# Kernel optimization log

Measured on AMD Instinct MI355X. Metric: run time of the kernel, lower is better.

The kernel has to match this reference:

```python
import jax, jax.numpy as jnp
import numpy as np
from jax import lax

B, N_ENT, D_ENT = 64, 512, 256
C_SCAT, C_MAP, W = 32, 18, 64
N_RES = 4


def conv2d(x, w, stride, pad):
    return lax.conv_general_dilated(x, w, (stride, stride), [(pad, pad), (pad, pad)],
                                    dimension_numbers=('NCHW', 'OIHW', 'NCHW'))


def batchnorm(x, g, b, eps=1e-5):
    # training-mode BN (batch statistics), matching nn.BatchNorm2d default train()
    mu = x.mean((0, 2, 3), keepdims=True)
    var = x.var((0, 2, 3), keepdims=True)
    return g[None, :, None, None] * (x - mu) * lax.rsqrt(var + eps) + b[None, :, None, None]


def setup_inputs() -> dict:
    key = jax.random.key(0)
    ks = jax.random.split(key, 24)
    s = 0.05
    inp = {
        'x': jax.random.uniform(ks[0], (B, C_MAP, W, W), jnp.float32),
        'entity_embeddings': jax.random.normal(ks[1], (B, N_ENT, D_ENT), jnp.float32),
        'entity_x_y': jax.random.randint(ks[2], (B, N_ENT, 16), 0, 2, jnp.int32),
        'conv1_w': jax.random.normal(ks[3], (C_SCAT, D_ENT), jnp.float32) * s,
        'project_w': jax.random.normal(ks[4], (32, C_SCAT + C_MAP, 1, 1), jnp.float32) * s,
        'project_b': jnp.zeros((32,), jnp.float32),
        'ds1_w': jax.random.normal(ks[5], (64, 32, 4, 4), jnp.float32) * s,
        'ds1_b': jnp.zeros((64,), jnp.float32),
        'ds2_w': jax.random.normal(ks[6], (128, 64, 4, 4), jnp.float32) * s,
        'ds2_b': jnp.zeros((128,), jnp.float32),
        'ds3_w': jax.random.normal(ks[7], (128, 128, 4, 4), jnp.float32) * s,
        'ds3_b': jnp.zeros((128,), jnp.float32),
        'res_conv1_w': jax.random.normal(ks[8], (N_RES, 128, 128, 3, 3), jnp.float32) * s,
        'res_bn1_g': jnp.ones((N_RES, 128), jnp.float32),
        'res_bn1_b': jnp.zeros((N_RES, 128), jnp.float32),
        'res_conv2_w': jax.random.normal(ks[9], (N_RES, 128, 128, 3, 3), jnp.float32) * s,
        'res_bn2_g': jnp.ones((N_RES, 128), jnp.float32),
        'res_bn2_b': jnp.zeros((N_RES, 128), jnp.float32),
        'fc_w': jax.random.normal(ks[10], (256, 8 * 8 * 128), jnp.float32) * s,
        'fc_b': jnp.zeros((256,), jnp.float32),
    }
    return inp


def _scatter(entity_embeddings, entity_x_y, conv1_w):
    # reduced = relu(Conv1d(256->32, k=1)) on entity dim
    reduced = jax.nn.relu(jnp.einsum('bnd,cd->bnc', entity_embeddings, conv1_w))  # [B,N,32]
    bits = entity_x_y
    pow2 = (2 ** jnp.arange(7, -1, -1)).astype(jnp.int32)
    xv = (bits[..., :8] * pow2).sum(-1) // 4   # [B,N] in 0..63
    yv = (bits[..., 8:] * pow2).sum(-1) // 4
    valid = (bits[..., 0] != -1000000000)
    reduced = reduced * valid[..., None].astype(reduced.dtype)
    b_idx = jnp.arange(entity_embeddings.shape[0], dtype=jnp.int32)[:, None]
    flat = (b_idx * (W * W) + yv * W + xv).reshape(-1)
    scat = jax.ops.segment_sum(reduced.reshape(-1, C_SCAT), flat, num_segments=entity_embeddings.shape[0] * W * W)
    return scat.reshape(-1, W, W, C_SCAT).transpose(0, 3, 1, 2)  # [B,32,W,W]


def reference(x, entity_embeddings, entity_x_y, conv1_w, project_w, project_b,
              ds1_w, ds1_b, ds2_w, ds2_b, ds3_w, ds3_b,
              res_conv1_w, res_bn1_g, res_bn1_b, res_conv2_w, res_bn2_g, res_bn2_b,
              fc_w, fc_b):
    scatter_map = _scatter(entity_embeddings, entity_x_y, conv1_w)
    h = jnp.concatenate([scatter_map, x], axis=1)  # [B,50,64,64]
    h = jax.nn.relu(conv2d(h, project_w, 1, 0) + project_b[None, :, None, None])
    h = jax.nn.relu(conv2d(h, ds1_w, 2, 1) + ds1_b[None, :, None, None])   # [B,64,32,32]
    h = jax.nn.relu(conv2d(h, ds2_w, 2, 1) + ds2_b[None, :, None, None])   # [B,128,16,16]
    h = jax.nn.relu(conv2d(h, ds3_w, 2, 1) + ds3_b[None, :, None, None])   # [B,128,8,8]
    map_skip = h
    for i in range(N_RES):
        identity = h
        o = batchnorm(conv2d(h, res_conv1_w[i], 1, 1), res_bn1_g[i], res_bn1_b[i])
        o = jax.nn.relu(o)
        o = batchnorm(conv2d(o, res_conv2_w[i], 1, 1), res_bn2_g[i], res_bn2_b[i])
        h = jax.nn.relu(o + identity)
        map_skip = map_skip + h
    flat = h.reshape(h.shape[0], -1)
    embedded_spatial = jax.nn.relu(flat @ fc_w.T + fc_b)
    return (map_skip, embedded_spatial)
```

## Files before the change

kernel.cpp:

```cpp
#include <hip/hip_runtime.h>
#include <hip/hip_bf16.h>

typedef __attribute__((ext_vector_type(8))) short bf16x8;
typedef __attribute__((ext_vector_type(4))) short bf16x4;
typedef __attribute__((ext_vector_type(4))) float f32x4;

__device__ __forceinline__ short f2bs(float v) {
  __hip_bfloat16 h = __float2bfloat16(v);
  return *reinterpret_cast<short*>(&h);
}

__global__ __launch_bounds__(256) void k_wall(
    const float* __restrict__ rc1w, const float* __restrict__ rc2w,
    const float* __restrict__ d1w, const float* __restrict__ d2w,
    const float* __restrict__ d3w, const float* __restrict__ fcw,
    const float* __restrict__ c1w, const float* __restrict__ pw,
    short* __restrict__ wTr1, short* __restrict__ wTr2, short* __restrict__ wTds1,
    short* __restrict__ wTds2, short* __restrict__ wTds3, short* __restrict__ wfcbf,
    short* __restrict__ wsc, short* __restrict__ wproj) {
  __shared__ float ld[128 * 65];
  const int bx = blockIdx.x;
  const int tid = threadIdx.x;
  if (bx < 4608) {
    const float* src = (bx < 2304) ? rc1w : rc2w;
    short* dst = (bx < 2304) ? wTr1 : wTr2;
    const int i = (bx % 2304) * 256 + tid;
    if (i < 589824) {
      const int layer = i / 147456;
      const int rem = i % 147456;
      const int tap = rem / 16384;
      const int r2 = rem & 16383;
      const int co = r2 >> 7, ci = r2 & 127;
      dst[i] = f2bs(src[(((size_t)layer * 16384 + co * 128 + ci) * 9) + tap]);
    }
  } else if (bx < 6272) {
    int CIN, n, base;
    const float* src;
    short* dst;
    if (bx < 4736) { CIN = 32; n = 32768; base = 4608; src = d1w; dst = wTds1; }
    else if (bx < 5248) { CIN = 64; n = 131072; base = 4736; src = d2w; dst = wTds2; }
    else { CIN = 128; n = 262144; base = 5248; src = d3w; dst = wTds3; }
    const int i = (bx - base) * 256 + tid;
    if (i < n) {
      const int COCI = n / 16;
      const int tap = i / COCI;
      const int rem = i % COCI;
      dst[i] = f2bs(src[(size_t)rem * 16 + tap]);
    }
  } else if (bx < 6528) {
    const int j = bx - 6272;
    const float* sp = fcw + (size_t)j * 8192;
    for (int i = tid; i < 8192; i += 256) {
      const int co = i >> 6, pix = i & 63;
      ld[co * 65 + pix] = sp[i];
    }
    __syncthreads();
    short* dp = wfcbf + (size_t)j * 8192;
    for (int i = tid; i < 8192; i += 256) {
      const int pix = i >> 7, co = i & 127;
      dp[i] = f2bs(ld[co * 65 + pix]);
    }
  } else if (bx < 6560) {
    const int i = (bx - 6528) * 256 + tid;
    if (i < 8192) wsc[i] = f2bs(c1w[i]);
  } else {
    const int i = (bx - 6560) * 256 + tid;
    if (i < 2048) {
      const int co = i >> 6, k = i & 63;
      wproj[i] = (k < 50) ? f2bs(pw[co * 50 + k]) : (short)0;
    }
  }
}

__global__ __launch_bounds__(256) void k_scatmfma(const float* __restrict__ emb,
                                                  const int* __restrict__ xy,
                                                  const short* __restrict__ wsc,
                                                  float* __restrict__ scat_pm) {
  constexpr int CIP = 264;
  __shared__ short abf[64 * CIP];
  __shared__ int flat[64];
  const int tid = threadIdx.x;
  const int e0 = blockIdx.x * 64;
  const float4* eg = (const float4*)(emb + (size_t)e0 * 256);
  for (int i = tid; i < 4096; i += 256) {
    const int e = i >> 6, k4 = i & 63;
    const float4 v = eg[(size_t)e * 64 + k4];
    bf16x4 o;
    o[0] = f2bs(v.x); o[1] = f2bs(v.y); o[2] = f2bs(v.z); o[3] = f2bs(v.w);
    *(bf16x4*)(&abf[e * CIP + k4 * 4]) = o;
  }
  if (tid < 64) {
    const int* bp = xy + (size_t)(e0 + tid) * 16;
    int xv = 0, yv = 0;
#pragma unroll
    for (int j = 0; j < 8; ++j) xv = (xv << 1) | bp[j];
#pragma unroll
    for (int j = 8; j < 16; ++j) yv = (yv << 1) | bp[j];
    flat[tid] = (bp[0] != -1000000000)
                    ? (((e0 + tid) >> 9) * 4096 + ((yv >> 2) << 6) + (xv >> 2))
                    : -1;
  }
  __syncthreads();
  const int wq = __builtin_amdgcn_readfirstlane(tid >> 6);
  const int lane = tid & 63;
  const int l15 = lane & 15, quad = lane >> 4;
  f32x4 acc[2];
  acc[0] = (f32x4){0.f, 0.f, 0.f, 0.f};
  acc[1] = (f32x4){0.f, 0.f, 0.f, 0.f};
  const short* arow = &abf[(wq * 16 + l15) * CIP + quad * 8];
  const short* w0 = wsc + (size_t)l15 * 256 + quad * 8;
  const short* w1 = wsc + (size_t)(16 + l15) * 256 + quad * 8;
#pragma unroll
  for (int kk = 0; kk < 8; ++kk) {
    bf16x8 a = *(const bf16x8*)(arow + kk * 32);
    acc[0] = __builtin_amdgcn_mfma_f32_16x16x32_bf16(a, *(const bf16x8*)(w0 + kk * 32), acc[0], 0, 0, 0);
    acc[1] = __builtin_amdgcn_mfma_f32_16x16x32_bf16(a, *(const bf16x8*)(w1 + kk * 32), acc[1], 0, 0, 0);
  }
#pragma unroll
  for (int nt = 0; nt < 2; ++nt)
#pragma unroll
    for (int r = 0; r < 4; ++r) {
      const int e = wq * 16 + quad * 4 + r;
      const float v = acc[nt][r];
      const int f = flat[e];
      if (f >= 0 && v > 0.f)
        atomicAdd(&scat_pm[(size_t)f * 32 + nt * 16 + l15], v);
    }
}

__global__ __launch_bounds__(256) void k_projmfma(const float* __restrict__ scat_pm,
                                                  const float* __restrict__ xin,
                                                  const short* __restrict__ wproj,
                                                  const float* __restrict__ pb,
                                                  short* __restrict__ h0pm) {
  constexpr int PK = 72;
  __shared__ short abf[128 * PK];
  const int tid = threadIdx.x;
  const int b = blockIdx.x >> 5;
  const int yx0 = (blockIdx.x & 31) << 7;
  const float4* sg = (const float4*)(scat_pm + ((size_t)(b * 4096 + yx0)) * 32);
  for (int i = tid; i < 1024; i += 256) {
    const int p = i >> 3, c4 = i & 7;
    const float4 v = sg[(size_t)p * 8 + c4];
    bf16x4 o;
    o[0] = f2bs(v.x); o[1] = f2bs(v.y); o[2] = f2bs(v.z); o[3] = f2bs(v.w);
    *(bf16x4*)(&abf[p * PK + c4 * 4]) = o;
  }
  for (int i = tid; i < 2304; i += 256) {
    const int run = i >> 7, p = i & 127;
    abf[p * PK + 32 + run] = f2bs(xin[(size_t)(b * 18 + run) * 4096 + yx0 + p]);
  }
  for (int i = tid; i < 2048; i += 256) {
    const int p = i >> 4, k = 50 + (i & 15);
    abf[p * PK + k] = 0;
  }
  __syncthreads();
  const int wq = __builtin_amdgcn_readfirstlane(tid >> 6);
  const int lane = tid & 63;
  const int l15 = lane & 15, quad = lane >> 4;
  f32x4 acc[2][2];
#pragma unroll
  for (int t = 0; t < 2; ++t)
#pragma unroll
    for (int n = 0; n < 2; ++n) acc[t][n] = (f32x4){0.f, 0.f, 0.f, 0.f};
  const short* wb0 = wproj + (size_t)l15 * 64 + quad * 8;
  const short* wb1 = wproj + (size_t)(16 + l15) * 64 + quad * 8;
#pragma unroll
  for (int kk = 0; kk < 2; ++kk) {
    const bf16x8 b0 = *(const bf16x8*)(wb0 + kk * 32);
    const bf16x8 b1 = *(const bf16x8*)(wb1 + kk * 32);
#pragma unroll
    for (int t = 0; t < 2; ++t) {
      const int pix = (wq * 2 + t) * 16 + l15;
      bf16x8 a = *(const bf16x8*)(&abf[pix * PK + quad * 8 + kk * 32]);
      acc[t][0] = __builtin_amdgcn_mfma_f32_16x16x32_bf16(a, b0, acc[t][0], 0, 0, 0);
      acc[t][1] = __builtin_amdgcn_mfma_f32_16x16x32_bf16(a, b1, acc[t][1], 0, 0, 0);
    }
  }
#pragma unroll
  for (int t = 0; t < 2; ++t)
#pragma unroll
    for (int n = 0; n < 2; ++n) {
      const int co = n * 16 + l15;
      const float bv = pb[co];
#pragma unroll
      for (int r = 0; r < 4; ++r) {
        const int pix = (wq * 2 + t) * 16 + quad * 4 + r;
        float v = acc[t][n][r] + bv;
        v = v > 0.f ? v : 0.f;
        h0pm[((size_t)(b * 4096 + yx0 + pix)) * 32 + co] = f2bs(v);
      }
    }
}

template <int CIN, int COUT, int HIN, int ROWSO, int COSPLIT, int MT, int NT, int OUTMODE>
__global__ __launch_bounds__(256) void k_ds2(const short* __restrict__ inpm,
                                             const short* __restrict__ wT,
                                             const float* __restrict__ bias,
                                             short* __restrict__ outbf,
                                             float* __restrict__ outf,
                                             float* __restrict__ msf) {
  constexpr int HOUT = HIN / 2;
  constexpr int ROWS = 2 * ROWSO + 2;
  constexpr int COLS = HIN + 2;
  constexpr int CHUNKS = CIN / 8;
  constexpr int KK = CIN / 32;
  constexpr int CIPAD = CIN + 8;
  constexpr int NHO = HOUT / ROWSO;
  __shared__ short lin[ROWS * COLS * CIPAD];
  const int tid = threadIdx.x;
  int bx = blockIdx.x;
  const int co_blk = (COSPLIT > 1) ? (bx % COSPLIT) : 0;
  if (COSPLIT > 1) bx /= COSPLIT;
  const int hoblk = bx % NHO;
  const int b = bx / NHO;
  for (int i = tid; i < ROWS * COLS * CHUNKS; i += 256) {
    const int ch = i % CHUNKS;
    const int pixv = i / CHUNKS;
    const int r = pixv / COLS, c = pixv % COLS;
    const int hi = 2 * ROWSO * hoblk - 1 + r;
    const int wc = c - 1;
    bf16x8 v = (bf16x8)(short)0;
    if (hi >= 0 && hi < HIN && wc >= 0 && wc < HIN)
      v = *(const bf16x8*)(inpm + ((size_t)(b * HIN + hi) * HIN + wc) * CIN + ch * 8);
    *(bf16x8*)(&lin[(r * COLS + c) * CIPAD + ch * 8]) = v;
  }
  __syncthreads();
  const int wq = __builtin_amdgcn_readfirstlane(tid >> 6);
  const int lane = tid & 63;
  const int l15 = lane & 15, quad = lane >> 4;
  const int mtile = (MT > 1) ? (wq % MT) : 0;
  const int cogrp = wq / MT;
  const int cobase = co_blk * (COUT / COSPLIT) + cogrp * (NT * 16);
  const int p = mtile * 16 + l15;
  const int dr = p / HOUT;
  const int col = p % HOUT;
  f32x4 acc[NT];
#pragma unroll
  for (int n = 0; n < NT; ++n) acc[n] = (f32x4){0.f, 0.f, 0.f, 0.f};
  const short* wrow = wT + (size_t)(cobase + l15) * CIN + quad * 8;
  for (int ky = 0; ky < 4; ++ky) {
    for (int kx = 0; kx < 4; ++kx) {
      const short* arow = &lin[((2 * dr + ky) * COLS + 2 * col + kx) * CIPAD + quad * 8];
      const short* wt = wrow + (size_t)(ky * 4 + kx) * COUT * CIN;
#pragma unroll
      for (int kk = 0; kk < KK; ++kk) {
        bf16x8 a = *(const bf16x8*)(arow + kk * 32);
#pragma unroll
        for (int n = 0; n < NT; ++n) {
          bf16x8 bf = *(const bf16x8*)(wt + n * 16 * CIN + kk * 32);
          acc[n] = __builtin_amdgcn_mfma_f32_16x16x32_bf16(a, bf, acc[n], 0, 0, 0);
        }
      }
    }
  }
#pragma unroll
  for (int n = 0; n < NT; ++n) {
    const int co = cobase + n * 16 + l15;
    const float bv = bias[co];
#pragma unroll
    for (int r = 0; r < 4; ++r) {
      const int pp = mtile * 16 + quad * 4 + r;
      const int dr2 = pp / HOUT;
      const int c2 = pp % HOUT;
      const int ho = hoblk * ROWSO + dr2;
      float v = acc[n][r] + bv;
      v = v > 0.f ? v : 0.f;
      const size_t o = ((size_t)b * HOUT * HOUT + ho * HOUT + c2) * COUT + co;
      outbf[o] = f2bs(v);
      if (OUTMODE == 1) {
        outf[o] = v;
        msf[o] = v;
      }
    }
  }
}

template <int BNIN>
__global__ __launch_bounds__(256) void k_resmfma(const short* __restrict__ hbfin,
                                                 const float* __restrict__ fin,
                                                 const float* __restrict__ statsIn,
                                                 const float* __restrict__ gIn,
                                                 const float* __restrict__ bIn,
                                                 const short* __restrict__ wT,
                                                 float* __restrict__ outpm,
                                                 float* __restrict__ statsOut) {
  constexpr int CIPAD = 136;
  __shared__ short lin[100 * CIPAD];
  __shared__ float bnsc[128], bnsh[128];
  const int tid = threadIdx.x;
  const int b = blockIdx.x >> 3;
  const int cobase = (blockIdx.x & 7) << 4;
  if (BNIN == 1) {
    if (tid < 128) {
      const float mu = statsIn[tid] * (1.f / 4096.f);
      const float var = statsIn[128 + tid] * (1.f / 4096.f) - mu * mu;
      const float sc = gIn[tid] * rsqrtf(var + 1e-5f);
      bnsc[tid] = sc;
      bnsh[tid] = bIn[tid] - mu * sc;
    }
    __syncthreads();
  }
  if (BNIN == 0) {
    const short* hb = hbfin + ((size_t)b << 13);
    for (int i = tid; i < 1600; i += 256) {
      const int pixel = i >> 4, ch = i & 15;
      const int r = pixel / 10, c = pixel % 10;
      bf16x8 v = (bf16x8)(short)0;
      if (r >= 1 && r <= 8 && c >= 1 && c <= 8)
        v = *(const bf16x8*)(hb + (((r - 1) << 3) + (c - 1)) * 128 + ch * 8);
      *(bf16x8*)(&lin[pixel * CIPAD + ch * 8]) = v;
    }
  } else {
    const float* fb = fin + ((size_t)b << 13);
    for (int i = tid; i < 3200; i += 256) {
      const int pixel = i >> 5, c4 = i & 31;
      const int r = pixel / 10, c = pixel % 10;
      bf16x4 o = (bf16x4)(short)0;
      if (r >= 1 && r <= 8 && c >= 1 && c <= 8) {
        const float4 x = *(const float4*)(fb + (size_t)(((r - 1) << 3) + (c - 1)) * 128 + c4 * 4);
        const float xv[4] = {x.x, x.y, x.z, x.w};
#pragma unroll
        for (int k = 0; k < 4; ++k) {
          const int ci = c4 * 4 + k;
          const float v = xv[k] * bnsc[ci] + bnsh[ci];
          o[k] = f2bs(v > 0.f ? v : 0.f);
        }
      }
      *(bf16x4*)(&lin[pixel * CIPAD + c4 * 4]) = o;
    }
  }
  __syncthreads();
  const int wq = __builtin_amdgcn_readfirstlane(tid >> 6);
  const int lane = tid & 63;
  const int l15 = lane & 15, quad = lane >> 4;
  const int p = wq * 16 + l15;
  const int py = p >> 3, px = p & 7;
  f32x4 acc = (f32x4){0.f, 0.f, 0.f, 0.f};
  const short* wrow = wT + (size_t)(cobase + l15) * 128 + quad * 8;
  for (int t = 0; t < 9; ++t) {
    const int ky = t / 3, kx = t % 3;
    const short* arow = &lin[((py + ky) * 10 + px + kx) * CIPAD + quad * 8];
    const short* wt = wrow + (size_t)t * 16384;
#pragma unroll
    for (int kk = 0; kk < 4; ++kk) {
      bf16x8 a = *(const bf16x8*)(arow + kk * 32);
      bf16x8 bf = *(const bf16x8*)(wt + kk * 32);
      acc = __builtin_amdgcn_mfma_f32_16x16x32_bf16(a, bf, acc, 0, 0, 0);
    }
  }
  float* ob = outpm + ((size_t)b << 13);
  const int co = cobase + l15;
  float s = 0.f, q = 0.f;
#pragma unroll
  for (int r = 0; r < 4; ++r) {
    const float v = acc[r];
    ob[(size_t)(wq * 16 + quad * 4 + r) * 128 + co] = v;
    s += v;
    q += v * v;
  }
  s += __shfl_down(s, 32); q += __shfl_down(q, 32);
  s += __shfl_down(s, 16); q += __shfl_down(q, 16);
  if (lane < 16) {
    atomicAdd(&statsOut[co], s);
    atomicAdd(&statsOut[128 + co], q);
  }
}

__global__ __launch_bounds__(256) void k_bnadd(const float* __restrict__ inpm,
                                               const float* __restrict__ stats,
                                               const float* __restrict__ g,
                                               const float* __restrict__ bb,
                                               const float* __restrict__ identpm,
                                               float* __restrict__ houtpm,
                                               short* __restrict__ houtbf,
                                               float* __restrict__ mspm) {
  const int idx = blockIdx.x * 256 + threadIdx.x;
  const int co = idx & 127;
  const float mu = stats[co] * (1.f / 4096.f);
  const float var = stats[128 + co] * (1.f / 4096.f) - mu * mu;
  float v = g[co] * (inpm[idx] - mu) * rsqrtf(var + 1e-5f) + bb[co];
  v += identpm[idx];
  v = v > 0.f ? v : 0.f;
  houtpm[idx] = v;
  houtbf[idx] = f2bs(v);
  mspm[idx] += v;
}

__global__ __launch_bounds__(256) void k_mstrans(const float* __restrict__ mspm,
                                                 float* __restrict__ out0) {
  __shared__ float t[64 * 132];
  const int b = blockIdx.x;
  const int tid = threadIdx.x;
  const float* sp = mspm + ((size_t)b << 13);
  for (int i = tid; i < 8192; i += 256) {
    const int pix = i >> 7, co = i & 127;
    t[pix * 132 + co] = sp[i];
  }
  __syncthreads();
  float* dp = out0 + ((size_t)b << 13);
  for (int i = tid; i < 8192; i += 256) {
    const int co = i >> 6, pix = i & 63;
    dp[i] = t[pix * 132 + co];
  }
}

__global__ __launch_bounds__(256) void k_fcmfma(const short* __restrict__ hbf,
                                                const short* __restrict__ wbf,
                                                float* __restrict__ part) {
  const int nb = blockIdx.x & 3;
  const int kb = blockIdx.x >> 2;
  const int wq = __builtin_amdgcn_readfirstlane((int)(threadIdx.x >> 6));
  const int lane = threadIdx.x & 63;
  const int l15 = lane & 15, quad = lane >> 4;
  const int k0 = kb * 256 + quad * 8;
  const short* wp = wbf + (size_t)(nb * 64 + wq * 16 + l15) * 8192 + k0;
  const short* hp = hbf + (size_t)l15 * 8192 + k0;
  f32x4 acc[4];
#pragma unroll
  for (int m = 0; m < 4; ++m) acc[m] = (f32x4){0.f, 0.f, 0.f, 0.f};
  for (int ks = 0; ks < 8; ++ks) {
    bf16x8 bfr = *(const bf16x8*)(wp + ks * 32);
#pragma unroll
    for (int m = 0; m < 4; ++m) {
      bf16x8 a = *(const bf16x8*)(hp + (size_t)m * 16 * 8192 + ks * 32);
      acc[m] = __builtin_amdgcn_mfma_f32_16x16x32_bf16(a, bfr, acc[m], 0, 0, 0);
    }
  }
#pragma unroll
  for (int m = 0; m < 4; ++m)
#pragma unroll
    for (int r = 0; r < 4; ++r) {
      const int b = m * 16 + quad * 4 + r;
      part[((size_t)kb * 64 + b) * 256 + nb * 64 + wq * 16 + l15] = acc[m][r];
    }
}

__global__ __launch_bounds__(256) void k_fcred(const float* __restrict__ part,
                                               const float* __restrict__ bias,
                                               float* __restrict__ out1) {
  const int idx = blockIdx.x * 256 + threadIdx.x;
  const int j = idx & 255;
  float s = 0.f;
#pragma unroll 8
  for (int kb = 0; kb < 32; ++kb) s += part[(size_t)kb * 16384 + idx];
  const float v = s + bias[j];
  out1[idx] = v > 0.f ? v : 0.f;
}

extern "C" void kernel_launch(void* const* d_in, const int* in_sizes, int n_in,
                              void* d_out, int out_size, void* d_ws, size_t ws_size,
                              hipStream_t stream) {
  const float* xin = (const float*)d_in[0];
  const float* emb = (const float*)d_in[1];
  const int* xy = (const int*)d_in[2];
  const float* c1w = (const float*)d_in[3];
  const float* pw = (const float*)d_in[4];
  const float* pb = (const float*)d_in[5];
  const float* d1w = (const float*)d_in[6];
  const float* d1b = (const float*)d_in[7];
  const float* d2w = (const float*)d_in[8];
  const float* d2b = (const float*)d_in[9];
  const float* d3w = (const float*)d_in[10];
  const float* d3b = (const float*)d_in[11];
  const float* rc1w = (const float*)d_in[12];
  const float* rbn1g = (const float*)d_in[13];
  const float* rbn1b = (const float*)d_in[14];
  const float* rc2w = (const float*)d_in[15];
  const float* rbn2g = (const float*)d_in[16];
  const float* rbn2b = (const float*)d_in[17];
  const float* fcw = (const float*)d_in[18];
  const float* fcb = (const float*)d_in[19];

  float* out0 = (float*)d_out;
  float* out1 = out0 + 524288;

  float* F = (float*)d_ws;
  float* scat = F + 0;
  float* h1pm_f = F + 0;
  float* h2pm_f = F + 2097152;
  float* hApm = F + 3145728;
  float* hBpm = F + 3670016;
  float* tmppm = F + 4194304;
  float* tmp2pm = F + 4718592;
  float* mspm = F + 5242880;
  short* pmbfA = (short*)(F + 5767168);
  short* pmbfB = (short*)(F + 6029312);
  float* stats = F + 6291456;
  float* fcpart = F + 6293504;
  short* h0pm = (short*)(F + 8388608);
  short* wfcbf = (short*)(F + 12582912);
  short* wTr1 = (short*)(F + 13631488);
  short* wTr2 = wTr1 + 589824;
  short* wTds1 = wTr2 + 589824;
  short* wTds2 = wTds1 + 32768;
  short* wTds3 = wTds2 + 131072;
  short* wsc = wTds3 + 262144;
  short* wproj = wsc + 8192;

  hipMemsetAsync(scat, 0, 8388608 * sizeof(float), stream);
  k_wall<<<6568, 256, 0, stream>>>(rc1w, rc2w, d1w, d2w, d3w, fcw, c1w, pw,
                                   wTr1, wTr2, wTds1, wTds2, wTds3, wfcbf, wsc, wproj);
  k_scatmfma<<<512, 256, 0, stream>>>(emb, xy, wsc, scat);
  k_projmfma<<<2048, 256, 0, stream>>>(scat, xin, wproj, pb, h0pm);
  hipMemsetAsync(stats, 0, 2048 * sizeof(float), stream);
  short* h1pm = (short*)h1pm_f;
  short* h2pm = (short*)h2pm_f;
  k_ds2<32, 64, 64, 2, 1, 4, 4, 0><<<1024, 256, 0, stream>>>(h0pm, wTds1, d1b, h1pm, hApm, mspm);
  k_ds2<64, 128, 32, 1, 1, 1, 2, 0><<<1024, 256, 0, stream>>>(h1pm, wTds2, d2b, h2pm, hApm, mspm);
  k_ds2<128, 128, 16, 2, 2, 1, 1, 1><<<512, 256, 0, stream>>>(h2pm, wTds3, d3b, pmbfA, hApm, mspm);

  float* cur = hApm;  float* nxt = hBpm;
  short* curbf = pmbfA; short* nxtbf = pmbfB;
  for (int i = 0; i < 4; ++i) {
    float* sA = stats + i * 512;
    float* sB = stats + i * 512 + 256;
    k_resmfma<0><<<512, 256, 0, stream>>>(curbf, nullptr, nullptr, nullptr, nullptr,
                                          wTr1 + (size_t)i * 147456, tmppm, sA);
    k_resmfma<1><<<512, 256, 0, stream>>>(nullptr, tmppm, sA, rbn1g + i * 128, rbn1b + i * 128,
                                          wTr2 + (size_t)i * 147456, tmp2pm, sB);
    k_bnadd<<<2048, 256, 0, stream>>>(tmp2pm, sB, rbn2g + i * 128, rbn2b + i * 128, cur, nxt,
                                      nxtbf, mspm);
    float* sw = cur; cur = nxt; nxt = sw;
    short* swb = curbf; curbf = nxtbf; nxtbf = swb;
  }
  k_mstrans<<<64, 256, 0, stream>>>(mspm, out0);
  k_fcmfma<<<128, 256, 0, stream>>>(curbf, wfcbf, fcpart);
  k_fcred<<<64, 256, 0, stream>>>(fcpart, fcb, out1);
}
```

Measured before the change: 409.5 us.

## Fuse downsample, residual, and FC stages into one persistent kernel with grid barriers

Replaces the chain of ds, resmfma, bnadd, mstrans and fc launches with a single persistent 512-block kernel. The stages are separated by atomic-counter grid barriers, and the residual identity and map_skip sums stay in registers. The BN2 output is applied straight from the accumulator, which drops the tmp2, bnadd and mstrans round trips and about twenty kernel launches. In exchange it relies on all 512 blocks being co-resident, which launch_bounds(256,2) is meant to allow, and it adds spin-wait barrier cost at each phase.

```diff
diff --git a/kernel.cpp b/kernel.cpp
--- a/kernel.cpp
+++ b/kernel.cpp
@@ -193,13 +193,24 @@
     }
 }
 
-template <int CIN, int COUT, int HIN, int ROWSO, int COSPLIT, int MT, int NT, int OUTMODE>
-__global__ __launch_bounds__(256) void k_ds2(const short* __restrict__ inpm,
-                                             const short* __restrict__ wT,
-                                             const float* __restrict__ bias,
-                                             short* __restrict__ outbf,
-                                             float* __restrict__ outf,
-                                             float* __restrict__ msf) {
+__device__ __forceinline__ void gbar(unsigned* cnt, unsigned target) {
+  __syncthreads();
+  if (threadIdx.x == 0) {
+    __threadfence();
+    __hip_atomic_fetch_add(cnt, 1u, __ATOMIC_RELEASE, __HIP_MEMORY_SCOPE_AGENT);
+    while (__hip_atomic_load(cnt, __ATOMIC_RELAXED, __HIP_MEMORY_SCOPE_AGENT) < target)
+      __builtin_amdgcn_s_sleep(1);
+    __threadfence();
+  }
+  __syncthreads();
+}
+
+template <int CIN, int COUT, int HIN, int ROWSO, int COSPLIT, int MT, int NT, int WRF32>
+__device__ __forceinline__ void ds2_phase(int bx, const short* __restrict__ inpm,
+                                          const short* __restrict__ wT,
+                                          const float* __restrict__ bias,
+                                          short* __restrict__ outbf,
+                                          float* __restrict__ outf, short* lin) {
   constexpr int HOUT = HIN / 2;
   constexpr int ROWS = 2 * ROWSO + 2;
   constexpr int COLS = HIN + 2;
@@ -207,13 +218,12 @@
   constexpr int KK = CIN / 32;
   constexpr int CIPAD = CIN + 8;
   constexpr int NHO = HOUT / ROWSO;
-  __shared__ short lin[ROWS * COLS * CIPAD];
   const int tid = threadIdx.x;
-  int bx = blockIdx.x;
   const int co_blk = (COSPLIT > 1) ? (bx % COSPLIT) : 0;
   if (COSPLIT > 1) bx /= COSPLIT;
   const int hoblk = bx % NHO;
   const int b = bx / NHO;
+  __syncthreads();
   for (int i = tid; i < ROWS * COLS * CHUNKS; i += 256) {
     const int ch = i % CHUNKS;
     const int pixv = i / CHUNKS;
@@ -268,79 +278,20 @@
       v = v > 0.f ? v : 0.f;
       const size_t o = ((size_t)b * HOUT * HOUT + ho * HOUT + c2) * COUT + co;
       outbf[o] = f2bs(v);
-      if (OUTMODE == 1) {
-        outf[o] = v;
-        msf[o] = v;
-      }
-    }
-  }
-}
-
-template <int BNIN>
-__global__ __launch_bounds__(256) void k_resmfma(const short* __restrict__ hbfin,
-                                                 const float* __restrict__ fin,
-                                                 const float* __restrict__ statsIn,
-                                                 const float* __restrict__ gIn,
-                                                 const float* __restrict__ bIn,
-                                                 const short* __restrict__ wT,
-                                                 float* __restrict__ outpm,
-                                                 float* __restrict__ statsOut) {
-  constexpr int CIPAD = 136;
-  __shared__ short lin[100 * CIPAD];
-  __shared__ float bnsc[128], bnsh[128];
-  const int tid = threadIdx.x;
-  const int b = blockIdx.x >> 3;
-  const int cobase = (blockIdx.x & 7) << 4;
-  if (BNIN == 1) {
-    if (tid < 128) {
-      const float mu = statsIn[tid] * (1.f / 4096.f);
-      const float var = statsIn[128 + tid] * (1.f / 4096.f) - mu * mu;
-      const float sc = gIn[tid] * rsqrtf(var + 1e-5f);
-      bnsc[tid] = sc;
-      bnsh[tid] = bIn[tid] - mu * sc;
-    }
-    __syncthreads();
-  }
-  if (BNIN == 0) {
-    const short* hb = hbfin + ((size_t)b << 13);
-    for (int i = tid; i < 1600; i += 256) {
-      const int pixel = i >> 4, ch = i & 15;
-      const int r = pixel / 10, c = pixel % 10;
-      bf16x8 v = (bf16x8)(short)0;
-      if (r >= 1 && r <= 8 && c >= 1 && c <= 8)
-        v = *(const bf16x8*)(hb + (((r - 1) << 3) + (c - 1)) * 128 + ch * 8);
-      *(bf16x8*)(&lin[pixel * CIPAD + ch * 8]) = v;
-    }
-  } else {
-    const float* fb = fin + ((size_t)b << 13);
-    for (int i = tid; i < 3200; i += 256) {
-      const int pixel = i >> 5, c4 = i & 31;
-      const int r = pixel / 10, c = pixel % 10;
-      bf16x4 o = (bf16x4)(short)0;
-      if (r >= 1 && r <= 8 && c >= 1 && c <= 8) {
-        const float4 x = *(const float4*)(fb + (size_t)(((r - 1) << 3) + (c - 1)) * 128 + c4 * 4);
-        const float xv[4] = {x.x, x.y, x.z, x.w};
-#pragma unroll
-        for (int k = 0; k < 4; ++k) {
-          const int ci = c4 * 4 + k;
-          const float v = xv[k] * bnsc[ci] + bnsh[ci];
-          o[k] = f2bs(v > 0.f ? v : 0.f);
-        }
-      }
-      *(bf16x4*)(&lin[pixel * CIPAD + c4 * 4]) = o;
-    }
-  }
-  __syncthreads();
-  const int wq = __builtin_amdgcn_readfirstlane(tid >> 6);
-  const int lane = tid & 63;
-  const int l15 = lane & 15, quad = lane >> 4;
+      if (WRF32) outf[o] = v;
+    }
+  }
+}
+
+__device__ __forceinline__ f32x4 res_mfma(const short* lin, const short* __restrict__ wT,
+                                          int cobase, int wq, int l15, int quad) {
   const int p = wq * 16 + l15;
   const int py = p >> 3, px = p & 7;
   f32x4 acc = (f32x4){0.f, 0.f, 0.f, 0.f};
   const short* wrow = wT + (size_t)(cobase + l15) * 128 + quad * 8;
   for (int t = 0; t < 9; ++t) {
     const int ky = t / 3, kx = t % 3;
-    const short* arow = &lin[((py + ky) * 10 + px + kx) * CIPAD + quad * 8];
+    const short* arow = &lin[((py + ky) * 10 + px + kx) * 136 + quad * 8];
     const short* wt = wrow + (size_t)t * 16384;
 #pragma unroll
     for (int kk = 0; kk < 4; ++kk) {
@@ -349,103 +300,173 @@
       acc = __builtin_amdgcn_mfma_f32_16x16x32_bf16(a, bf, acc, 0, 0, 0);
     }
   }
-  float* ob = outpm + ((size_t)b << 13);
+  return acc;
+}
+
+__global__ __launch_bounds__(256, 2) void k_tail(
+    const short* __restrict__ h0pm,
+    const short* __restrict__ wTds1, const float* __restrict__ d1b, short* __restrict__ h1pm,
+    const short* __restrict__ wTds2, const float* __restrict__ d2b, short* __restrict__ h2pm,
+    const short* __restrict__ wTds3, const float* __restrict__ d3b,
+    short* __restrict__ hbf, float* __restrict__ hf32, float* __restrict__ tmppm,
+    const short* __restrict__ wTr1, const short* __restrict__ wTr2,
+    const float* __restrict__ rbn1g, const float* __restrict__ rbn1b,
+    const float* __restrict__ rbn2g, const float* __restrict__ rbn2b,
+    float* __restrict__ stats, unsigned* __restrict__ cnt,
+    const short* __restrict__ wfc, const float* __restrict__ fcb,
+    float* __restrict__ fcpart, float* __restrict__ out0, float* __restrict__ out1) {
+  __shared__ short smem[15840];
+  const int bid = blockIdx.x;
+  const int tid = threadIdx.x;
+  unsigned ph = 0;
+
+  ds2_phase<32, 64, 64, 2, 1, 4, 4, 0>(bid, h0pm, wTds1, d1b, h1pm, nullptr, smem);
+  ds2_phase<32, 64, 64, 2, 1, 4, 4, 0>(bid + 512, h0pm, wTds1, d1b, h1pm, nullptr, smem);
+  gbar(cnt, 512u * (++ph));
+  ds2_phase<64, 128, 32, 1, 1, 1, 2, 0>(bid, h1pm, wTds2, d2b, h2pm, nullptr, smem);
+  ds2_phase<64, 128, 32, 1, 1, 1, 2, 0>(bid + 512, h1pm, wTds2, d2b, h2pm, nullptr, smem);
+  gbar(cnt, 512u * (++ph));
+  ds2_phase<128, 128, 16, 2, 2, 1, 1, 1>(bid, h2pm, wTds3, d3b, hbf, hf32, smem);
+  gbar(cnt, 512u * (++ph));
+
+  const int b = bid >> 3;
+  const int cobase = (bid & 7) << 4;
+  const int wq = __builtin_amdgcn_readfirstlane(tid >> 6);
+  const int lane = tid & 63;
+  const int l15 = lane & 15, quad = lane >> 4;
   const int co = cobase + l15;
-  float s = 0.f, q = 0.f;
-#pragma unroll
-  for (int r = 0; r < 4; ++r) {
-    const float v = acc[r];
-    ob[(size_t)(wq * 16 + quad * 4 + r) * 128 + co] = v;
-    s += v;
-    q += v * v;
-  }
-  s += __shfl_down(s, 32); q += __shfl_down(q, 32);
-  s += __shfl_down(s, 16); q += __shfl_down(q, 16);
-  if (lane < 16) {
-    atomicAdd(&statsOut[co], s);
-    atomicAdd(&statsOut[128 + co], q);
-  }
-}
-
-__global__ __launch_bounds__(256) void k_bnadd(const float* __restrict__ inpm,
-                                               const float* __restrict__ stats,
-                                               const float* __restrict__ g,
-                                               const float* __restrict__ bb,
-                                               const float* __restrict__ identpm,
-                                               float* __restrict__ houtpm,
-                                               short* __restrict__ houtbf,
-                                               float* __restrict__ mspm) {
-  const int idx = blockIdx.x * 256 + threadIdx.x;
-  const int co = idx & 127;
-  const float mu = stats[co] * (1.f / 4096.f);
-  const float var = stats[128 + co] * (1.f / 4096.f) - mu * mu;
-  float v = g[co] * (inpm[idx] - mu) * rsqrtf(var + 1e-5f) + bb[co];
-  v += identpm[idx];
-  v = v > 0.f ? v : 0.f;
-  houtpm[idx] = v;
-  houtbf[idx] = f2bs(v);
-  mspm[idx] += v;
-}
-
-__global__ __launch_bounds__(256) void k_mstrans(const float* __restrict__ mspm,
-                                                 float* __restrict__ out0) {
-  __shared__ float t[64 * 132];
-  const int b = blockIdx.x;
-  const int tid = threadIdx.x;
-  const float* sp = mspm + ((size_t)b << 13);
-  for (int i = tid; i < 8192; i += 256) {
-    const int pix = i >> 7, co = i & 127;
-    t[pix * 132 + co] = sp[i];
-  }
-  __syncthreads();
-  float* dp = out0 + ((size_t)b << 13);
-  for (int i = tid; i < 8192; i += 256) {
-    const int co = i >> 6, pix = i & 63;
-    dp[i] = t[pix * 132 + co];
-  }
-}
-
-__global__ __launch_bounds__(256) void k_fcmfma(const short* __restrict__ hbf,
-                                                const short* __restrict__ wbf,
-                                                float* __restrict__ part) {
-  const int nb = blockIdx.x & 3;
-  const int kb = blockIdx.x >> 2;
-  const int wq = __builtin_amdgcn_readfirstlane((int)(threadIdx.x >> 6));
-  const int lane = threadIdx.x & 63;
-  const int l15 = lane & 15, quad = lane >> 4;
-  const int k0 = kb * 256 + quad * 8;
-  const short* wp = wbf + (size_t)(nb * 64 + wq * 16 + l15) * 8192 + k0;
-  const short* hp = hbf + (size_t)l15 * 8192 + k0;
-  f32x4 acc[4];
-#pragma unroll
-  for (int m = 0; m < 4; ++m) acc[m] = (f32x4){0.f, 0.f, 0.f, 0.f};
-  for (int ks = 0; ks < 8; ++ks) {
-    bf16x8 bfr = *(const bf16x8*)(wp + ks * 32);
-#pragma unroll
-    for (int m = 0; m < 4; ++m) {
-      bf16x8 a = *(const bf16x8*)(hp + (size_t)m * 16 * 8192 + ks * 32);
-      acc[m] = __builtin_amdgcn_mfma_f32_16x16x32_bf16(a, bfr, acc[m], 0, 0, 0);
-    }
-  }
-#pragma unroll
-  for (int m = 0; m < 4; ++m)
+  float hloc[4], msloc[4];
+  {
+    const float* hf = hf32 + ((size_t)b << 13);
 #pragma unroll
     for (int r = 0; r < 4; ++r) {
-      const int b = m * 16 + quad * 4 + r;
-      part[((size_t)kb * 64 + b) * 256 + nb * 64 + wq * 16 + l15] = acc[m][r];
-    }
-}
-
-__global__ __launch_bounds__(256) void k_fcred(const float* __restrict__ part,
-                                               const float* __restrict__ bias,
-                                               float* __restrict__ out1) {
-  const int idx = blockIdx.x * 256 + threadIdx.x;
-  const int j = idx & 255;
-  float s = 0.f;
+      hloc[r] = hf[(size_t)(wq * 16 + quad * 4 + r) * 128 + co];
+      msloc[r] = hloc[r];
+    }
+  }
+  float* const bnsc = (float*)(smem + 13600);
+  float* const bnsh = bnsc + 128;
+
+  for (int i = 0; i < 4; ++i) {
+    float* sA = stats + i * 512;
+    float* sB = sA + 256;
+    {
+      __syncthreads();
+      const short* hb = hbf + ((size_t)b << 13);
+      for (int t = tid; t < 1600; t += 256) {
+        const int pixel = t >> 4, ch = t & 15;
+        const int r = pixel / 10, c = pixel % 10;
+        bf16x8 v = (bf16x8)(short)0;
+        if (r >= 1 && r <= 8 && c >= 1 && c <= 8)
+          v = *(const bf16x8*)(hb + (((r - 1) << 3) + (c - 1)) * 128 + ch * 8);
+        *(bf16x8*)(&smem[pixel * 136 + ch * 8]) = v;
+      }
+      __syncthreads();
+      f32x4 acc = res_mfma(smem, wTr1 + (size_t)i * 147456, cobase, wq, l15, quad);
+      float* ob = tmppm + ((size_t)b << 13);
+      float s = 0.f, q = 0.f;
+#pragma unroll
+      for (int r = 0; r < 4; ++r) {
+        const float v = acc[r];
+        ob[(size_t)(wq * 16 + quad * 4 + r) * 128 + co] = v;
+        s += v; q += v * v;
+      }
+      s += __shfl_down(s, 32); q += __shfl_down(q, 32);
+      s += __shfl_down(s, 16); q += __shfl_down(q, 16);
+      if (lane < 16) {
+        atomicAdd(&sA[cobase + lane], s);
+        atomicAdd(&sA[128 + cobase + lane], q);
+      }
+    }
+    gbar(cnt, 512u * (++ph));
+    f32x4 acc2;
+    {
+      __syncthreads();
+      if (tid < 128) {
+        const float mu = sA[tid] * (1.f / 4096.f);
+        const float var = sA[128 + tid] * (1.f / 4096.f) - mu * mu;
+        const float sc = rbn1g[i * 128 + tid] * rsqrtf(var + 1e-5f);
+        bnsc[tid] = sc;
+        bnsh[tid] = rbn1b[i * 128 + tid] - mu * sc;
+      }
+      __syncthreads();
+      const float* fb = tmppm + ((size_t)b << 13);
+      for (int t = tid; t < 3200; t += 256) {
+        const int pixel = t >> 5, c4 = t & 31;
+        const int r = pixel / 10, c = pixel % 10;
+        bf16x4 o = (bf16x4)(short)0;
+        if (r >= 1 && r <= 8 && c >= 1 && c <= 8) {
+          const float4 x = *(const float4*)(fb + (size_t)(((r - 1) << 3) + (c - 1)) * 128 + c4 * 4);
+          const float xv[4] = {x.x, x.y, x.z, x.w};
+#pragma unroll
+          for (int k2 = 0; k2 < 4; ++k2) {
+            const int ci = c4 * 4 + k2;
+            const float v = xv[k2] * bnsc[ci] + bnsh[ci];
+            o[k2] = f2bs(v > 0.f ? v : 0.f);
+          }
+        }
+        *(bf16x4*)(&smem[pixel * 136 + c4 * 4]) = o;
+      }
+      __syncthreads();
+      acc2 = res_mfma(smem, wTr2 + (size_t)i * 147456, cobase, wq, l15, quad);
+      float s = 0.f, q = 0.f;
+#pragma unroll
+      for (int r = 0; r < 4; ++r) { s += acc2[r]; q += acc2[r] * acc2[r]; }
+      s += __shfl_down(s, 32); q += __shfl_down(q, 32);
+      s += __shfl_down(s, 16); q += __shfl_down(q, 16);
+      if (lane < 16) {
+        atomicAdd(&sB[cobase + lane], s);
+        atomicAdd(&sB[128 + cobase + lane], q);
+      }
+    }
+    gbar(cnt, 512u * (++ph));
+    {
+      const float mu = sB[co] * (1.f / 4096.f);
+      const float var = sB[128 + co] * (1.f / 4096.f) - mu * mu;
+      const float sc = rbn2g[i * 128 + co] * rsqrtf(var + 1e-5f);
+      const float sh = rbn2b[i * 128 + co] - mu * sc;
+      short* hb = hbf + ((size_t)b << 13);
+#pragma unroll
+      for (int r = 0; r < 4; ++r) {
+        float v = acc2[r] * sc + sh + hloc[r];
+        v = v > 0.f ? v : 0.f;
+        hloc[r] = v;
+        msloc[r] += v;
+        hb[(size_t)(wq * 16 + quad * 4 + r) * 128 + co] = f2bs(v);
+      }
+    }
+    gbar(cnt, 512u * (++ph));
+  }
+
+  {
+    float* ob = out0 + ((size_t)b << 13) + (size_t)co * 64;
+#pragma unroll
+    for (int r = 0; r < 4; ++r) ob[wq * 16 + quad * 4 + r] = msloc[r];
+  }
+
+  {
+    const int kb = bid >> 4, jb = bid & 15;
+    const int k0 = kb * 256 + quad * 8;
+    const short* hp = hbf + (size_t)(wq * 16 + l15) * 8192 + k0;
+    const short* wp = wfc + (size_t)(jb * 16 + l15) * 8192 + k0;
+    f32x4 acc = (f32x4){0.f, 0.f, 0.f, 0.f};
+#pragma unroll
+    for (int ks = 0; ks < 8; ++ks)
+      acc = __builtin_amdgcn_mfma_f32_16x16x32_bf16(*(const bf16x8*)(hp + ks * 32),
+                                                    *(const bf16x8*)(wp + ks * 32), acc, 0, 0, 0);
+#pragma unroll
+    for (int r = 0; r < 4; ++r)
+      fcpart[((size_t)kb * 64 + wq * 16 + quad * 4 + r) * 256 + jb * 16 + l15] = acc[r];
+  }
+  gbar(cnt, 512u * (++ph));
+  if (bid < 64) {
+    const int idx = bid * 256 + tid;
+    float s = 0.f;
 #pragma unroll 8
-  for (int kb = 0; kb < 32; ++kb) s += part[(size_t)kb * 16384 + idx];
-  const float v = s + bias[j];
-  out1[idx] = v > 0.f ? v : 0.f;
+    for (int kb2 = 0; kb2 < 32; ++kb2) s += fcpart[(size_t)kb2 * 16384 + idx];
+    const float v = s + fcb[idx & 255];
+    out1[idx] = v > 0.f ? v : 0.f;
+  }
 }
 
 extern "C" void kernel_launch(void* const* d_in, const int* in_sizes, int n_in,
@@ -477,17 +498,14 @@
 
   float* F = (float*)d_ws;
   float* scat = F + 0;
-  float* h1pm_f = F + 0;
-  float* h2pm_f = F + 2097152;
-  float* hApm = F + 3145728;
-  float* hBpm = F + 3670016;
+  short* h1pm = (short*)(F + 0);
+  short* h2pm = (short*)(F + 2097152);
+  float* hf32 = F + 3145728;
   float* tmppm = F + 4194304;
-  float* tmp2pm = F + 4718592;
-  float* mspm = F + 5242880;
-  short* pmbfA = (short*)(F + 5767168);
-  short* pmbfB = (short*)(F + 6029312);
+  short* hbf = (short*)(F + 5767168);
   float* stats = F + 6291456;
-  float* fcpart = F + 6293504;
+  unsigned* cnt = (unsigned*)(F + 6293504);
+  float* fcpart = F + 6293568;
   short* h0pm = (short*)(F + 8388608);
   short* wfcbf = (short*)(F + 12582912);
   short* wTr1 = (short*)(F + 13631488);
@@ -503,28 +521,8 @@
                                    wTr1, wTr2, wTds1, wTds2, wTds3, wfcbf, wsc, wproj);
   k_scatmfma<<<512, 256, 0, stream>>>(emb, xy, wsc, scat);
   k_projmfma<<<2048, 256, 0, stream>>>(scat, xin, wproj, pb, h0pm);
-  hipMemsetAsync(stats, 0, 2048 * sizeof(float), stream);
-  short* h1pm = (short*)h1pm_f;
-  short* h2pm = (short*)h2pm_f;
-  k_ds2<32, 64, 64, 2, 1, 4, 4, 0><<<1024, 256, 0, stream>>>(h0pm, wTds1, d1b, h1pm, hApm, mspm);
-  k_ds2<64, 128, 32, 1, 1, 1, 2, 0><<<1024, 256, 0, stream>>>(h1pm, wTds2, d2b, h2pm, hApm, mspm);
-  k_ds2<128, 128, 16, 2, 2, 1, 1, 1><<<512, 256, 0, stream>>>(h2pm, wTds3, d3b, pmbfA, hApm, mspm);
-
-  float* cur = hApm;  float* nxt = hBpm;
-  short* curbf = pmbfA; short* nxtbf = pmbfB;
-  for (int i = 0; i < 4; ++i) {
-    float* sA = stats + i * 512;
-    float* sB = stats + i * 512 + 256;
-    k_resmfma<0><<<512, 256, 0, stream>>>(curbf, nullptr, nullptr, nullptr, nullptr,
-                                          wTr1 + (size_t)i * 147456, tmppm, sA);
-    k_resmfma<1><<<512, 256, 0, stream>>>(nullptr, tmppm, sA, rbn1g + i * 128, rbn1b + i * 128,
-                                          wTr2 + (size_t)i * 147456, tmp2pm, sB);
-    k_bnadd<<<2048, 256, 0, stream>>>(tmp2pm, sB, rbn2g + i * 128, rbn2b + i * 128, cur, nxt,
-                                      nxtbf, mspm);
-    float* sw = cur; cur = nxt; nxt = sw;
-    short* swb = curbf; curbf = nxtbf; nxtbf = swb;
-  }
-  k_mstrans<<<64, 256, 0, stream>>>(mspm, out0);
-  k_fcmfma<<<128, 256, 0, stream>>>(curbf, wfcbf, fcpart);
-  k_fcred<<<64, 256, 0, stream>>>(fcpart, fcb, out1);
-}
+  hipMemsetAsync(stats, 0, (2048 + 16) * sizeof(float), stream);
+  k_tail<<<512, 256, 0, stream>>>(h0pm, wTds1, d1b, h1pm, wTds2, d2b, h2pm, wTds3, d3b,
+                                  hbf, hf32, tmppm, wTr1, wTr2, rbn1g, rbn1b, rbn2g, rbn2b,
+                                  stats, cnt, wfcbf, fcb, fcpart, out0, out1);
+}
```

Result: slower. 1.256 ms (+206.8%).

## Fuse residual BN-add into next conv and fold memsets into weight prep

Applied to the files above, without the earlier changes.

Folds the two hipMemsetAsync calls into extra blocks of the weight-conversion kernel. The separate BN2+residual+ReLU kernel is fused into the next block's first 3x3 conv, which now applies BN2 while staging its halo tile into LDS. The final BN-add is fused into the map_skip transpose kernel, which also emits the bf16 input for the FC. The aim is fewer launches and less round-trip global traffic. In exchange, each conv block recomputes the BN-add for its whole image tile, and ownership of the fp32 writes is split across the 8 channel blocks.

```diff
diff --git a/kernel.cpp b/kernel.cpp
--- a/kernel.cpp
+++ b/kernel.cpp
@@ -17,7 +17,8 @@
     const float* __restrict__ c1w, const float* __restrict__ pw,
     short* __restrict__ wTr1, short* __restrict__ wTr2, short* __restrict__ wTds1,
     short* __restrict__ wTds2, short* __restrict__ wTds3, short* __restrict__ wfcbf,
-    short* __restrict__ wsc, short* __restrict__ wproj) {
+    short* __restrict__ wsc, short* __restrict__ wproj,
+    float* __restrict__ scatz, float* __restrict__ statsz) {
   __shared__ float ld[128 * 65];
   const int bx = blockIdx.x;
   const int tid = threadIdx.x;
@@ -63,12 +64,18 @@
   } else if (bx < 6560) {
     const int i = (bx - 6528) * 256 + tid;
     if (i < 8192) wsc[i] = f2bs(c1w[i]);
-  } else {
+  } else if (bx < 6568) {
     const int i = (bx - 6560) * 256 + tid;
     if (i < 2048) {
       const int co = i >> 6, k = i & 63;
       wproj[i] = (k < 50) ? f2bs(pw[co * 50 + k]) : (short)0;
     }
+  } else if (bx < 7080) {
+    float4* dst = (float4*)(scatz + (size_t)(bx - 6568) * 16384);
+    const float4 z = {0.f, 0.f, 0.f, 0.f};
+    for (int t = tid; t < 4096; t += 256) dst[t] = z;
+  } else {
+    for (int i = tid; i < 2064; i += 256) statsz[i] = 0.f;
   }
 }
 
@@ -367,41 +374,129 @@
   }
 }
 
-__global__ __launch_bounds__(256) void k_bnadd(const float* __restrict__ inpm,
-                                               const float* __restrict__ stats,
-                                               const float* __restrict__ g,
-                                               const float* __restrict__ bb,
-                                               const float* __restrict__ identpm,
-                                               float* __restrict__ houtpm,
-                                               short* __restrict__ houtbf,
-                                               float* __restrict__ mspm) {
-  const int idx = blockIdx.x * 256 + threadIdx.x;
-  const int co = idx & 127;
-  const float mu = stats[co] * (1.f / 4096.f);
-  const float var = stats[128 + co] * (1.f / 4096.f) - mu * mu;
-  float v = g[co] * (inpm[idx] - mu) * rsqrtf(var + 1e-5f) + bb[co];
-  v += identpm[idx];
-  v = v > 0.f ? v : 0.f;
-  houtpm[idx] = v;
-  houtbf[idx] = f2bs(v);
-  mspm[idx] += v;
-}
-
-__global__ __launch_bounds__(256) void k_mstrans(const float* __restrict__ mspm,
-                                                 float* __restrict__ out0) {
+__global__ __launch_bounds__(256) void k_resA(const float* __restrict__ tmp2,
+                                              const float* __restrict__ statsB,
+                                              const float* __restrict__ g2,
+                                              const float* __restrict__ b2,
+                                              const float* __restrict__ identf,
+                                              float* __restrict__ houtf,
+                                              float* __restrict__ mspm,
+                                              const short* __restrict__ wT,
+                                              float* __restrict__ outpm,
+                                              float* __restrict__ statsOut) {
+  constexpr int CIPAD = 136;
+  __shared__ short lin[100 * CIPAD];
+  __shared__ float bnsc[128], bnsh[128];
+  const int tid = threadIdx.x;
+  const int b = blockIdx.x >> 3;
+  const int cobase = (blockIdx.x & 7) << 4;
+  if (tid < 128) {
+    const float mu = statsB[tid] * (1.f / 4096.f);
+    const float var = statsB[128 + tid] * (1.f / 4096.f) - mu * mu;
+    const float sc = g2[tid] * rsqrtf(var + 1e-5f);
+    bnsc[tid] = sc;
+    bnsh[tid] = b2[tid] - mu * sc;
+  }
+  __syncthreads();
+  const float* fb = tmp2 + ((size_t)b << 13);
+  const float* idb = identf + ((size_t)b << 13);
+  for (int t = tid; t < 3200; t += 256) {
+    const int pixel = t >> 5, c4 = t & 31;
+    const int r = pixel / 10, c = pixel % 10;
+    bf16x4 o = (bf16x4)(short)0;
+    if (r >= 1 && r <= 8 && c >= 1 && c <= 8) {
+      const size_t p8 = (size_t)(((r - 1) << 3) + (c - 1)) * 128 + c4 * 4;
+      const float4 x = *(const float4*)(fb + p8);
+      const float4 id = *(const float4*)(idb + p8);
+      const float xv[4] = {x.x, x.y, x.z, x.w};
+      const float iv[4] = {id.x, id.y, id.z, id.w};
+#pragma unroll
+      for (int k = 0; k < 4; ++k) {
+        const int ci = c4 * 4 + k;
+        const float v = xv[k] * bnsc[ci] + bnsh[ci] + iv[k];
+        o[k] = f2bs(v > 0.f ? v : 0.f);
+      }
+    }
+    *(bf16x4*)(&lin[pixel * CIPAD + c4 * 4]) = o;
+  }
+  for (int t = tid; t < 1024; t += 256) {
+    const int pix = t >> 4, cl = t & 15;
+    const int cow = cobase + cl;
+    const size_t o = ((size_t)b << 13) + (size_t)pix * 128 + cow;
+    float v = tmp2[o] * bnsc[cow] + bnsh[cow] + identf[o];
+    v = v > 0.f ? v : 0.f;
+    houtf[o] = v;
+    mspm[o] += v;
+  }
+  __syncthreads();
+  const int wq = __builtin_amdgcn_readfirstlane(tid >> 6);
+  const int lane = tid & 63;
+  const int l15 = lane & 15, quad = lane >> 4;
+  const int p = wq * 16 + l15;
+  const int py = p >> 3, px = p & 7;
+  f32x4 acc = (f32x4){0.f, 0.f, 0.f, 0.f};
+  const short* wrow = wT + (size_t)(cobase + l15) * 128 + quad * 8;
+  for (int t = 0; t < 9; ++t) {
+    const int ky = t / 3, kx = t % 3;
+    const short* arow = &lin[((py + ky) * 10 + px + kx) * CIPAD + quad * 8];
+    const short* wt = wrow + (size_t)t * 16384;
+#pragma unroll
+    for (int kk = 0; kk < 4; ++kk) {
+      bf16x8 a = *(const bf16x8*)(arow + kk * 32);
+      bf16x8 bf = *(const bf16x8*)(wt + kk * 32);
+      acc = __builtin_amdgcn_mfma_f32_16x16x32_bf16(a, bf, acc, 0, 0, 0);
+    }
+  }
+  float* ob = outpm + ((size_t)b << 13);
+  const int co = cobase + l15;
+  float s = 0.f, q = 0.f;
+#pragma unroll
+  for (int r = 0; r < 4; ++r) {
+    const float v = acc[r];
+    ob[(size_t)(wq * 16 + quad * 4 + r) * 128 + co] = v;
+    s += v;
+    q += v * v;
+  }
+  s += __shfl_down(s, 32); q += __shfl_down(q, 32);
+  s += __shfl_down(s, 16); q += __shfl_down(q, 16);
+  if (lane < 16) {
+    atomicAdd(&statsOut[co], s);
+    atomicAdd(&statsOut[128 + co], q);
+  }
+}
+
+__global__ __launch_bounds__(256) void k_msfin(const float* __restrict__ tmp2,
+                                               const float* __restrict__ statsB,
+                                               const float* __restrict__ g2,
+                                               const float* __restrict__ b2,
+                                               const float* __restrict__ identf,
+                                               const float* __restrict__ mspm,
+                                               short* __restrict__ hbf,
+                                               float* __restrict__ out0) {
   __shared__ float t[64 * 132];
+  __shared__ float bnsc[128], bnsh[128];
   const int b = blockIdx.x;
   const int tid = threadIdx.x;
-  const float* sp = mspm + ((size_t)b << 13);
+  if (tid < 128) {
+    const float mu = statsB[tid] * (1.f / 4096.f);
+    const float var = statsB[128 + tid] * (1.f / 4096.f) - mu * mu;
+    const float sc = g2[tid] * rsqrtf(var + 1e-5f);
+    bnsc[tid] = sc;
+    bnsh[tid] = b2[tid] - mu * sc;
+  }
+  __syncthreads();
+  const size_t base = (size_t)b << 13;
   for (int i = tid; i < 8192; i += 256) {
     const int pix = i >> 7, co = i & 127;
-    t[pix * 132 + co] = sp[i];
-  }
-  __syncthreads();
-  float* dp = out0 + ((size_t)b << 13);
+    float v = tmp2[base + i] * bnsc[co] + bnsh[co] + identf[base + i];
+    v = v > 0.f ? v : 0.f;
+    hbf[base + i] = f2bs(v);
+    t[pix * 132 + co] = mspm[base + i] + v;
+  }
+  __syncthreads();
   for (int i = tid; i < 8192; i += 256) {
     const int co = i >> 6, pix = i & 63;
-    dp[i] = t[pix * 132 + co];
+    out0[base + i] = t[pix * 132 + co];
   }
 }
 
@@ -477,15 +572,15 @@
 
   float* F = (float*)d_ws;
   float* scat = F + 0;
-  float* h1pm_f = F + 0;
-  float* h2pm_f = F + 2097152;
+  short* h1pm = (short*)(F + 0);
+  short* h2pm = (short*)(F + 2097152);
   float* hApm = F + 3145728;
   float* hBpm = F + 3670016;
   float* tmppm = F + 4194304;
   float* tmp2pm = F + 4718592;
   float* mspm = F + 5242880;
   short* pmbfA = (short*)(F + 5767168);
-  short* pmbfB = (short*)(F + 6029312);
+  short* hbf = (short*)(F + 6029312);
   float* stats = F + 6291456;
   float* fcpart = F + 6293504;
   short* h0pm = (short*)(F + 8388608);
@@ -498,33 +593,34 @@
   short* wsc = wTds3 + 262144;
   short* wproj = wsc + 8192;
 
-  hipMemsetAsync(scat, 0, 8388608 * sizeof(float), stream);
-  k_wall<<<6568, 256, 0, stream>>>(rc1w, rc2w, d1w, d2w, d3w, fcw, c1w, pw,
-                                   wTr1, wTr2, wTds1, wTds2, wTds3, wfcbf, wsc, wproj);
+  k_wall<<<7081, 256, 0, stream>>>(rc1w, rc2w, d1w, d2w, d3w, fcw, c1w, pw,
+                                   wTr1, wTr2, wTds1, wTds2, wTds3, wfcbf, wsc, wproj,
+                                   scat, stats);
   k_scatmfma<<<512, 256, 0, stream>>>(emb, xy, wsc, scat);
   k_projmfma<<<2048, 256, 0, stream>>>(scat, xin, wproj, pb, h0pm);
-  hipMemsetAsync(stats, 0, 2048 * sizeof(float), stream);
-  short* h1pm = (short*)h1pm_f;
-  short* h2pm = (short*)h2pm_f;
-  k_ds2<32, 64, 64, 2, 1, 4, 4, 0><<<1024, 256, 0, stream>>>(h0pm, wTds1, d1b, h1pm, hApm, mspm);
-  k_ds2<64, 128, 32, 1, 1, 1, 2, 0><<<1024, 256, 0, stream>>>(h1pm, wTds2, d2b, h2pm, hApm, mspm);
+  k_ds2<32, 64, 64, 2, 1, 4, 4, 0><<<1024, 256, 0, stream>>>(h0pm, wTds1, d1b, h1pm, nullptr, nullptr);
+  k_ds2<64, 128, 32, 1, 1, 1, 2, 0><<<1024, 256, 0, stream>>>(h1pm, wTds2, d2b, h2pm, nullptr, nullptr);
   k_ds2<128, 128, 16, 2, 2, 1, 1, 1><<<512, 256, 0, stream>>>(h2pm, wTds3, d3b, pmbfA, hApm, mspm);
 
-  float* cur = hApm;  float* nxt = hBpm;
-  short* curbf = pmbfA; short* nxtbf = pmbfB;
-  for (int i = 0; i < 4; ++i) {
-    float* sA = stats + i * 512;
-    float* sB = stats + i * 512 + 256;
-    k_resmfma<0><<<512, 256, 0, stream>>>(curbf, nullptr, nullptr, nullptr, nullptr,
-                                          wTr1 + (size_t)i * 147456, tmppm, sA);
-    k_resmfma<1><<<512, 256, 0, stream>>>(nullptr, tmppm, sA, rbn1g + i * 128, rbn1b + i * 128,
-                                          wTr2 + (size_t)i * 147456, tmp2pm, sB);
-    k_bnadd<<<2048, 256, 0, stream>>>(tmp2pm, sB, rbn2g + i * 128, rbn2b + i * 128, cur, nxt,
-                                      nxtbf, mspm);
-    float* sw = cur; cur = nxt; nxt = sw;
-    short* swb = curbf; curbf = nxtbf; nxtbf = swb;
-  }
-  k_mstrans<<<64, 256, 0, stream>>>(mspm, out0);
-  k_fcmfma<<<128, 256, 0, stream>>>(curbf, wfcbf, fcpart);
+  k_resmfma<0><<<512, 256, 0, stream>>>(pmbfA, nullptr, nullptr, nullptr, nullptr,
+                                        wTr1, tmppm, stats);
+  k_resmfma<1><<<512, 256, 0, stream>>>(nullptr, tmppm, stats, rbn1g, rbn1b,
+                                        wTr2, tmp2pm, stats + 256);
+  float* idp = hApm;
+  float* hop = hBpm;
+  for (int i = 1; i < 4; ++i) {
+    k_resA<<<512, 256, 0, stream>>>(tmp2pm, stats + (i - 1) * 512 + 256,
+                                    rbn2g + (i - 1) * 128, rbn2b + (i - 1) * 128,
+                                    idp, hop, mspm, wTr1 + (size_t)i * 147456,
+                                    tmppm, stats + i * 512);
+    k_resmfma<1><<<512, 256, 0, stream>>>(nullptr, tmppm, stats + i * 512,
+                                          rbn1g + i * 128, rbn1b + i * 128,
+                                          wTr2 + (size_t)i * 147456, tmp2pm,
+                                          stats + i * 512 + 256);
+    float* sw = idp; idp = hop; hop = sw;
+  }
+  k_msfin<<<64, 256, 0, stream>>>(tmp2pm, stats + 3 * 512 + 256, rbn2g + 3 * 128,
+                                  rbn2b + 3 * 128, idp, mspm, hbf, out0);
+  k_fcmfma<<<128, 256, 0, stream>>>(hbf, wfcbf, fcpart);
   k_fcred<<<64, 256, 0, stream>>>(fcpart, fcb, out1);
 }
```

Result: no change. 404.4 us (-1.2%).
